# Kernel tuning notes

Measured on AMD Instinct MI355X. Metric: run time of the kernel, lower is better.

Reference implementation:

```python
import jax, jax.numpy as jnp
import numpy as np

N, F_IN, H1, H2 = 8192, 512, 256, 128
EPS_VAR = 1e-6


def setup_inputs() -> dict:
    key = jax.random.key(0)
    ks = jax.random.split(key, 12)
    rn = lambda k, s, sc=1.0: jax.random.normal(k, s, dtype=jnp.float32) * sc
    x = rn(ks[0], (N, F_IN))
    # dense normalized-adjacency surrogate: row sums ~0.5 keep activations bounded
    adj = jax.random.uniform(ks[1], (N, N), dtype=jnp.float32) / N
    g = lambda k, fi, fo: rn(k, (fi, fo), (1.0 / fi) ** 0.5)
    W1 = g(ks[2], F_IN, H1)
    W2 = g(ks[3], H1, H2)
    W3 = g(ks[4], H1, H2)
    W4 = g(ks[5], H1, H2)
    W5 = g(ks[6], H1, H2)
    Wl = g(ks[7], 2 * H2, H2)
    bl = jnp.zeros((H2,), jnp.float32)
    eps_z = rn(ks[8], (N, H2))          # eps for reparameterize (N(0,1))
    eps_group = rn(ks[9], (1, H2), 0.1)  # group eps ~ N(0, 0.1)
    batch = jnp.zeros((N,), jnp.int32)   # torch code uses all-ones labels -> one group
    return dict(x=x, adj=adj, W1=W1, W2=W2, W3=W3, W4=W4, W5=W5,
                Wl=Wl, bl=bl, eps_z=eps_z, eps_group=eps_group, batch=batch)


def _gcn(adj, h, W, act):
    return act(adj @ (h @ W))


def _accumulate_group_evidence(clz_mu, clz_logvar, batch):
    # precision-weighted group mean/var, vectorized segment reduce (1 group here)
    var = jnp.exp(clz_logvar)
    var = jnp.where(var == 0.0, EPS_VAR, var)
    inv = 1.0 / var                                             # [N,H2]
    prec = jax.ops.segment_sum(inv, batch, num_segments=1)      # [G,H2]
    gvar = 1.0 / prec
    gmu = gvar * jax.ops.segment_sum(clz_mu * inv, batch, num_segments=1)
    grouped_mu = gmu[batch]                                     # [N,H2]
    gv = gvar[batch]
    gv = jnp.where(gv == 0.0, EPS_VAR, gv)
    return grouped_mu, jnp.log(gv)


def reference(x, adj, W1, W2, W3, W4, W5, Wl, bl, eps_z, eps_group, batch):
    h1 = _gcn(adj, x, W1, jax.nn.relu)
    ident = lambda v: v
    mu = _gcn(adj, h1, W2, ident)
    logvar = _gcn(adj, h1, W3, ident)
    clz_mu = _gcn(adj, h1, W4, ident)
    clz_logvar = _gcn(adj, h1, W5, ident)

    # reparameterize: std = exp(logvar) in the original (no 0.5 factor)
    z = eps_z * jnp.exp(logvar) + mu

    # group evidence path uses .data in torch -> detached from encoder
    grouped_mu, grouped_logvar = _accumulate_group_evidence(
        jax.lax.stop_gradient(clz_mu), jax.lax.stop_gradient(clz_logvar), batch)

    # group-wise reparameterize: same eps per group, std = exp(0.5*logvar)
    class_lat = grouped_mu + jnp.exp(0.5 * grouped_logvar) * eps_group[batch]

    updated_z = jnp.concatenate([z, class_lat], axis=-1) @ Wl + bl  # [N,H2]
    adj_recon = updated_z @ updated_z.T                             # [N,N], act=identity
    return adj_recon, z, mu, logvar, grouped_mu, grouped_logvar
```

## Files before the change

### kernel.cpp

```cpp
#include <hip/hip_runtime.h>
#include <math.h>
#include <stdint.h>

namespace {

constexpr long OUT_ADJ = 0;
constexpr long OUT_Z   = 67108864;
constexpr long OUT_MU  = 68157440;
constexpr long OUT_LV  = 69206016;
constexpr long OUT_GMU = 70254592;
constexpr long OUT_GLV = 71303168;

constexpr long P_F32OFF    = 0;
constexpr long ADJBF_U16   = 16777216;
constexpr long Y1T_U16     = 83886080;
constexpr long H1T_U16     = 85983232;

constexpr long OFF_Y1    = 0;
constexpr long OFF_U     = 0;
constexpr long OFF_UBF   = 1048576;
constexpr long OFF_STATS = 1572864;
constexpr long OFF_G     = 2097152;
constexpr long OFF_M2    = 4194304;
constexpr long OFF_WCAT  = 8388608;

typedef short bf16x8 __attribute__((ext_vector_type(8)));
typedef float f32x4  __attribute__((ext_vector_type(4)));

__device__ __forceinline__ uint16_t f2bf(float f) {
    uint32_t u = __float_as_uint(f);
    return (uint16_t)((u + 0x7FFFu + ((u >> 16) & 1u)) >> 16);
}

__device__ __forceinline__ void gload16(const void* g, void* lds) {
    __builtin_amdgcn_global_load_lds(
        (__attribute__((address_space(1))) void*)(void*)g,
        (__attribute__((address_space(3))) void*)lds, 16, 0, 0);
}

__global__ __launch_bounds__(256)
void cast_bf16(const float* __restrict__ in, uint16_t* __restrict__ out, long n8) {
    long i = (long)blockIdx.x * 256 + threadIdx.x;
    if (i >= n8) return;
    const float4* p = (const float4*)in + i * 2;
    float4 a = p[0], b = p[1];
    union { uint16_t u[8]; uint4 v; } r;
    r.u[0] = f2bf(a.x); r.u[1] = f2bf(a.y); r.u[2] = f2bf(a.z); r.u[3] = f2bf(a.w);
    r.u[4] = f2bf(b.x); r.u[5] = f2bf(b.y); r.u[6] = f2bf(b.z); r.u[7] = f2bf(b.w);
    *(uint4*)(out + i * 8) = r.v;
}

__global__ __launch_bounds__(256)
void pack_wcat(const float* __restrict__ W2, const float* __restrict__ W3,
               const float* __restrict__ W4, const float* __restrict__ W5,
               float* __restrict__ Wcat) {
    int id = blockIdx.x * 256 + threadIdx.x;
    int k = id >> 9;
    int c = id & 511;
    int q = c >> 7, cc = c & 127;
    const float* W = (q == 0) ? W2 : (q == 1) ? W3 : (q == 2) ? W4 : W5;
    Wcat[id] = W[k * 128 + cc];
}

__global__ void init_stats(float* stats) {
    int t = threadIdx.x;
    if (t < 256) stats[t] = 0.f;
}

template<bool RELU, bool BIAS>
__global__ __launch_bounds__(256)
void gemm128x64(const float* __restrict__ A, const float* __restrict__ B,
                const float* __restrict__ bias, float* __restrict__ C,
                int M, int N, int K) {
    constexpr int SA = 132;
    constexpr int SB = 68;
    __shared__ float Ast[16 * SA];
    __shared__ float Bs[16 * SB];
    const int t  = threadIdx.x;
    const int tx = t & 15, ty = t >> 4;
    const long i0 = (long)blockIdx.x * 128;
    const long j0 = (long)blockIdx.y * 64;

    const int a_row = t >> 2;
    const int a_q   = (t & 3) << 2;
    const int b_k   = t >> 4;
    const int b_c   = (t & 15) << 2;

    const float* Ap0 = A + (i0 + a_row) * (long)K + a_q;
    const float* Ap1 = Ap0 + 64l * K;
    const float* Bp  = B + (long)b_k * N + j0 + b_c;

    float acc[8][4] = {};

    for (int kt = 0; kt < K; kt += 16) {
        float4 av0 = *(const float4*)(Ap0 + kt);
        float4 av1 = *(const float4*)(Ap1 + kt);
        float4 bv  = *(const float4*)(Bp + (long)kt * N);
        __syncthreads();
        Ast[(a_q + 0) * SA + a_row] = av0.x;
        Ast[(a_q + 1) * SA + a_row] = av0.y;
        Ast[(a_q + 2) * SA + a_row] = av0.z;
        Ast[(a_q + 3) * SA + a_row] = av0.w;
        Ast[(a_q + 0) * SA + a_row + 64] = av1.x;
        Ast[(a_q + 1) * SA + a_row + 64] = av1.y;
        Ast[(a_q + 2) * SA + a_row + 64] = av1.z;
        Ast[(a_q + 3) * SA + a_row + 64] = av1.w;
        *(float4*)&Bs[b_k * SB + b_c] = bv;
        __syncthreads();
        #pragma unroll
        for (int k = 0; k < 16; ++k) {
            float a[8], b[4];
            *(float4*)&a[0] = *(const float4*)&Ast[k * SA + ty * 8];
            *(float4*)&a[4] = *(const float4*)&Ast[k * SA + ty * 8 + 4];
            *(float4*)&b[0] = *(const float4*)&Bs[k * SB + tx * 4];
            #pragma unroll
            for (int ii = 0; ii < 8; ++ii)
                #pragma unroll
                for (int jj = 0; jj < 4; ++jj)
                    acc[ii][jj] = fmaf(a[ii], b[jj], acc[ii][jj]);
        }
    }

    #pragma unroll
    for (int ii = 0; ii < 8; ++ii) {
        long gi = i0 + ty * 8 + ii;
        float4 v;
        float* vp = &v.x;
        #pragma unroll
        for (int jj = 0; jj < 4; ++jj) {
            float xv = acc[ii][jj];
            if (BIAS) xv += bias[j0 + tx * 4 + jj];
            if (RELU) xv = fmaxf(xv, 0.f);
            vp[jj] = xv;
        }
        *(float4*)&C[gi * N + j0 + tx * 4] = v;
    }
}

__global__ __launch_bounds__(256)
void gemm_mfma_bt(const uint16_t* __restrict__ A, const uint16_t* __restrict__ BT,
                  float* __restrict__ P, int ldx, int Nout, int Ksplit) {
    __shared__ uint16_t sA[128 * 64];
    __shared__ uint16_t sB[128 * 64];
    const int t = threadIdx.x;
    const int l = t & 63, w = t >> 6;
    const int quad = l >> 4, l15 = l & 15;
    const long i0 = (long)blockIdx.x * 128;
    const long j0 = (long)blockIdx.y * 128;
    const int kbase = blockIdx.z * Ksplit;

    const uint16_t* gA[4];
    const uint16_t* gB[4];
    int dstb[4];
    #pragma unroll
    for (int q = 0; q < 4; ++q) {
        int cid = (q * 4 + w) * 64 + l;
        int row = cid >> 3;
        int cg  = (cid & 7) ^ (row & 7);
        gA[q] = A  + (i0 + row) * (long)ldx + kbase + cg * 8;
        gB[q] = BT + (j0 + row) * (long)ldx + kbase + cg * 8;
        dstb[q] = (q * 4 + w) * 1024;
    }

    const int wm = w & 1, wn = w >> 1;
    int offA[2][4], offB[2][4];
    #pragma unroll
    for (int ks = 0; ks < 2; ++ks) {
        int g = ks * 4 + quad;
        #pragma unroll
        for (int i = 0; i < 4; ++i) {
            int m = 64 * wm + 16 * i + l15;
            offA[ks][i] = m * 64 + ((g ^ (m & 7)) * 8);
            int n = 64 * wn + 16 * i + l15;
            offB[ks][i] = n * 64 + ((g ^ (n & 7)) * 8);
        }
    }

    f32x4 acc[4][4];
    #pragma unroll
    for (int i = 0; i < 4; ++i)
        #pragma unroll
        for (int j = 0; j < 4; ++j)
            acc[i][j] = (f32x4){0.f, 0.f, 0.f, 0.f};

    char* sAb = (char*)&sA[0];
    char* sBb = (char*)&sB[0];
    for (int kt = 0; kt < Ksplit; kt += 64) {
        __syncthreads();
        #pragma unroll
        for (int q = 0; q < 4; ++q) {
            gload16(gA[q] + kt, sAb + dstb[q]);
            gload16(gB[q] + kt, sBb + dstb[q]);
        }
        __syncthreads();
        #pragma unroll
        for (int ks = 0; ks < 2; ++ks) {
            bf16x8 af[4], bfr[4];
            #pragma unroll
            for (int mi = 0; mi < 4; ++mi) af[mi]  = *(const bf16x8*)&sA[offA[ks][mi]];
            #pragma unroll
            for (int ni = 0; ni < 4; ++ni) bfr[ni] = *(const bf16x8*)&sB[offB[ks][ni]];
            #pragma unroll
            for (int mi = 0; mi < 4; ++mi)
                #pragma unroll
                for (int ni = 0; ni < 4; ++ni)
                    acc[mi][ni] = __builtin_amdgcn_mfma_f32_16x16x32_bf16(
                        af[mi], bfr[ni], acc[mi][ni], 0, 0, 0);
        }
    }

    float* Pz = P + (long)blockIdx.z * (8192l * Nout);
    #pragma unroll
    for (int mi = 0; mi < 4; ++mi) {
        #pragma unroll
        for (int ni = 0; ni < 4; ++ni) {
            f32x4 v = acc[mi][ni];
            long col = j0 + 64 * wn + 16 * ni + l15;
            #pragma unroll
            for (int r = 0; r < 4; ++r) {
                long row = i0 + 64 * wm + 16 * mi + quad * 4 + r;
                Pz[row * Nout + col] = v[r];
            }
        }
    }
}

template<int NSUM, bool RELU>
__global__ __launch_bounds__(256)
void reduce_transpose_cast(const float* __restrict__ P, int M, int Ncols, long stride,
                           uint16_t* __restrict__ OT) {
    __shared__ float tile[64][65];
    long r0 = (long)blockIdx.x * 64;
    int  c0 = blockIdx.y * 64;
    int t = threadIdx.x;
    #pragma unroll
    for (int p = 0; p < 16; ++p) {
        int e = p * 256 + t;
        int r = e >> 6, c = e & 63;
        long idx = (r0 + r) * Ncols + c0 + c;
        float s = 0.f;
        #pragma unroll
        for (int q = 0; q < NSUM; ++q) s += P[idx + q * stride];
        if (RELU) s = fmaxf(s, 0.f);
        tile[r][c] = s;
    }
    __syncthreads();
    #pragma unroll
    for (int p = 0; p < 16; ++p) {
        int e = p * 256 + t;
        int c = e >> 6, r = e & 63;
        OT[(long)(c0 + c) * M + r0 + r] = f2bf(tile[r][c]);
    }
}

__global__ __launch_bounds__(256)
void reduce4(const float4* __restrict__ P, float4* __restrict__ G) {
    long i = (long)blockIdx.x * 256 + threadIdx.x;
    float4 a = P[i], b = P[i + 524288], c = P[i + 1048576], d = P[i + 1572864];
    float4 r;
    r.x = a.x + b.x + c.x + d.x;
    r.y = a.y + b.y + c.y + d.y;
    r.z = a.z + b.z + c.z + d.z;
    r.w = a.w + b.w + c.w + d.w;
    G[i] = r;
}

__global__ __launch_bounds__(128)
void group_reduce(const float* __restrict__ M2, float* __restrict__ stats) {
    int j = threadIdx.x;
    long base = (long)blockIdx.x * 32;
    float accP = 0.f, accS = 0.f;
    for (int r = 0; r < 32; ++r) {
        long i = base + r;
        float cmu = M2[i * 512 + 256 + j];
        float clv = M2[i * 512 + 384 + j];
        float var = expf(clv);
        if (var == 0.f) var = 1e-6f;
        float inv = 1.f / var;
        accP += inv;
        accS += cmu * inv;
    }
    atomicAdd(&stats[j], accP);
    atomicAdd(&stats[128 + j], accS);
}

__global__ __launch_bounds__(128)
void finalize_k(float* __restrict__ stats, const float* __restrict__ eps_group,
                const float* __restrict__ Wl, const float* __restrict__ bl) {
    __shared__ float cl[128];
    int j = threadIdx.x;
    float prec = stats[j];
    float s    = stats[128 + j];
    float gvar = 1.f / prec;
    float gmu  = gvar * s;
    float gv   = gvar; if (gv == 0.f) gv = 1e-6f;
    float glv  = logf(gv);
    stats[256 + j] = gmu;
    stats[384 + j] = glv;
    cl[j] = gmu + expf(0.5f * glv) * eps_group[j];
    __syncthreads();
    float c2 = bl[j];
    for (int k = 0; k < 128; ++k)
        c2 = fmaf(cl[k], Wl[(128 + k) * 128 + j], c2);
    stats[512 + j] = c2;
}

__global__ __launch_bounds__(256)
void epilogue_z(const float* __restrict__ M2, const float* __restrict__ eps_z,
                const float* __restrict__ stats, float* __restrict__ out) {
    long id = (long)blockIdx.x * 256 + threadIdx.x;
    long i = id >> 7;
    int  j = (int)(id & 127);
    float mu = M2[i * 512 + j];
    float lv = M2[i * 512 + 128 + j];
    out[OUT_Z   + id] = eps_z[id] * expf(lv) + mu;
    out[OUT_MU  + id] = mu;
    out[OUT_LV  + id] = lv;
    out[OUT_GMU + id] = stats[256 + j];
    out[OUT_GLV + id] = stats[384 + j];
}

__global__ __launch_bounds__(256)
void aat_mfma(const uint16_t* __restrict__ U, float* __restrict__ C) {
    __shared__ uint16_t sA[128 * 128];
    __shared__ uint16_t sB[128 * 128];
    const int t = threadIdx.x;
    const int l = t & 63, w = t >> 6;
    const int quad = l >> 4, l15 = l & 15;
    const long i0 = (long)blockIdx.x * 128;
    const long j0 = (long)blockIdx.y * 128;

    #pragma unroll
    for (int q = 0; q < 8; ++q) {
        int cid = (q * 4 + w) * 64 + l;
        int row = cid >> 4;
        int cg  = (cid & 15) ^ (row & 15);
        int dstb = (q * 4 + w) * 1024;
        gload16(U + (i0 + row) * 128 + cg * 8, (char*)&sA[0] + dstb);
        gload16(U + (j0 + row) * 128 + cg * 8, (char*)&sB[0] + dstb);
    }

    f32x4 acc[4][4];
    #pragma unroll
    for (int i = 0; i < 4; ++i)
        #pragma unroll
        for (int j = 0; j < 4; ++j)
            acc[i][j] = (f32x4){0.f, 0.f, 0.f, 0.f};

    __syncthreads();

    const int wm = w & 1, wn = w >> 1;
    #pragma unroll
    for (int ks = 0; ks < 4; ++ks) {
        int g = ks * 4 + quad;
        bf16x8 af[4], bfr[4];
        #pragma unroll
        for (int mi = 0; mi < 4; ++mi) {
            int m = 64 * wm + 16 * mi + l15;
            af[mi] = *(const bf16x8*)&sA[m * 128 + ((g ^ (m & 15)) * 8)];
        }
        #pragma unroll
        for (int ni = 0; ni < 4; ++ni) {
            int n = 64 * wn + 16 * ni + l15;
            bfr[ni] = *(const bf16x8*)&sB[n * 128 + ((g ^ (n & 15)) * 8)];
        }
        #pragma unroll
        for (int mi = 0; mi < 4; ++mi)
            #pragma unroll
            for (int ni = 0; ni < 4; ++ni)
                acc[mi][ni] = __builtin_amdgcn_mfma_f32_16x16x32_bf16(
                    af[mi], bfr[ni], acc[mi][ni], 0, 0, 0);
    }

    #pragma unroll
    for (int mi = 0; mi < 4; ++mi) {
        #pragma unroll
        for (int ni = 0; ni < 4; ++ni) {
            f32x4 v = acc[mi][ni];
            long col = j0 + 64 * wn + 16 * ni + l15;
            #pragma unroll
            for (int r = 0; r < 4; ++r) {
                long row = i0 + 64 * wm + 16 * mi + quad * 4 + r;
                C[row * 8192 + col] = v[r];
            }
        }
    }
}

}

extern "C" void kernel_launch(void* const* d_in, const int* in_sizes, int n_in,
                              void* d_out, int out_size, void* d_ws, size_t ws_size,
                              hipStream_t stream) {
    (void)in_sizes; (void)n_in; (void)out_size; (void)ws_size;
    const float* x     = (const float*)d_in[0];
    const float* adj   = (const float*)d_in[1];
    const float* W1    = (const float*)d_in[2];
    const float* W2    = (const float*)d_in[3];
    const float* W3    = (const float*)d_in[4];
    const float* W4    = (const float*)d_in[5];
    const float* W5    = (const float*)d_in[6];
    const float* Wl    = (const float*)d_in[7];
    const float* bl    = (const float*)d_in[8];
    const float* eps_z = (const float*)d_in[9];
    const float* eps_g = (const float*)d_in[10];

    float*    out  = (float*)d_out;
    uint16_t* outu = (uint16_t*)d_out;
    float*    ws   = (float*)d_ws;

    float*    P     = out + P_F32OFF;
    uint16_t* adjbf = outu + ADJBF_U16;
    uint16_t* Y1T   = outu + Y1T_U16;
    uint16_t* h1T   = outu + H1T_U16;

    float*    Y1  = ws + OFF_Y1;
    float*    U   = ws + OFF_U;
    uint16_t* Ubf = (uint16_t*)(ws + OFF_UBF);
    float*    st  = ws + OFF_STATS;
    float*    G   = ws + OFF_G;
    float*    M2  = ws + OFF_M2;
    float*    Wc  = ws + OFF_WCAT;

    cast_bf16<<<32768, 256, 0, stream>>>(adj, adjbf, 8388608);
    pack_wcat<<<512, 256, 0, stream>>>(W2, W3, W4, W5, Wc);
    init_stats<<<1, 256, 0, stream>>>(st);

    gemm128x64<false, false><<<dim3(64, 4), 256, 0, stream>>>(x, W1, nullptr, Y1, 8192, 256, 512);
    reduce_transpose_cast<1, false><<<dim3(128, 4), 256, 0, stream>>>(Y1, 8192, 256, 0, Y1T);

    gemm_mfma_bt<<<dim3(64, 2, 4), 256, 0, stream>>>(adjbf, Y1T, P, 8192, 256, 2048);
    reduce_transpose_cast<4, true><<<dim3(128, 4), 256, 0, stream>>>(P, 8192, 256, 2097152, h1T);

    gemm_mfma_bt<<<dim3(64, 2, 4), 256, 0, stream>>>(adjbf, h1T, P, 8192, 256, 2048);
    reduce4<<<2048, 256, 0, stream>>>((const float4*)P, (float4*)G);

    gemm128x64<false, false><<<dim3(64, 8), 256, 0, stream>>>(G, Wc, nullptr, M2, 8192, 512, 256);

    group_reduce<<<256, 128, 0, stream>>>(M2, st);
    finalize_k<<<1, 128, 0, stream>>>(st, eps_g, Wl, bl);
    epilogue_z<<<4096, 256, 0, stream>>>(M2, eps_z, st, out);

    gemm128x64<false, true><<<dim3(64, 2), 256, 0, stream>>>(out + OUT_Z, Wl, st + 512, U, 8192, 128, 128);
    cast_bf16<<<512, 256, 0, stream>>>(U, Ubf, 131072);

    aat_mfma<<<dim3(64, 64), 256, 0, stream>>>(Ubf, out);
}
```

Baseline: 791.6 us.

## Replace fp32 SIMT GEMMs with bf16 MFMA GEMMs and fuse weight prep

The three small fp32 FMA GEMMs (x@W1, G@Wcat, z@Wl) become instances of the bf16 MFMA kernel, which gains epilogue modes for transposed bf16 output and bias plus bf16 output. Weight transposes/casts, the x cast and the stats init are merged into one prep kernel. The reduce and epilogue kernels now emit bf16 directly, removing the separate transpose-cast and cast passes. These GEMMs are small next to the adjacency GEMMs, so the overall gain is limited, and bf16 inputs add rounding error to mu/logvar and the reconstruction.

Result: faster. 693.5 us (-12.4%).

```diff
diff --git a/kernel.cpp b/kernel.cpp
--- a/kernel.cpp
+++ b/kernel.cpp
@@ -15,14 +15,16 @@
 constexpr long ADJBF_U16   = 16777216;
 constexpr long Y1T_U16     = 83886080;
 constexpr long H1T_U16     = 85983232;
-
-constexpr long OFF_Y1    = 0;
-constexpr long OFF_U     = 0;
+constexpr long XBF_U16     = 88080384;
+constexpr long GBF_U16     = 92274688;
+constexpr long ZBF_U16     = 94371840;
+constexpr long W1T_U16     = 95420416;
+constexpr long WCT_U16     = 95551488;
+constexpr long WLT_U16     = 95682560;
+
 constexpr long OFF_UBF   = 1048576;
 constexpr long OFF_STATS = 1572864;
-constexpr long OFF_G     = 2097152;
 constexpr long OFF_M2    = 4194304;
-constexpr long OFF_WCAT  = 8388608;
 
 typedef short bf16x8 __attribute__((ext_vector_type(8)));
 typedef float f32x4  __attribute__((ext_vector_type(4)));
@@ -51,95 +53,48 @@
 }
 
 __global__ __launch_bounds__(256)
-void pack_wcat(const float* __restrict__ W2, const float* __restrict__ W3,
-               const float* __restrict__ W4, const float* __restrict__ W5,
-               float* __restrict__ Wcat) {
-    int id = blockIdx.x * 256 + threadIdx.x;
-    int k = id >> 9;
-    int c = id & 511;
-    int q = c >> 7, cc = c & 127;
-    const float* W = (q == 0) ? W2 : (q == 1) ? W3 : (q == 2) ? W4 : W5;
-    Wcat[id] = W[k * 128 + cc];
-}
-
-__global__ void init_stats(float* stats) {
+void prep_small(const float* __restrict__ x, const float* __restrict__ W1,
+                const float* __restrict__ W2, const float* __restrict__ W3,
+                const float* __restrict__ W4, const float* __restrict__ W5,
+                const float* __restrict__ Wl,
+                uint16_t* __restrict__ xbf, uint16_t* __restrict__ W1T,
+                uint16_t* __restrict__ WcT, uint16_t* __restrict__ WlT,
+                float* __restrict__ stats) {
+    int b = blockIdx.x;
     int t = threadIdx.x;
-    if (t < 256) stats[t] = 0.f;
-}
-
-template<bool RELU, bool BIAS>
-__global__ __launch_bounds__(256)
-void gemm128x64(const float* __restrict__ A, const float* __restrict__ B,
-                const float* __restrict__ bias, float* __restrict__ C,
-                int M, int N, int K) {
-    constexpr int SA = 132;
-    constexpr int SB = 68;
-    __shared__ float Ast[16 * SA];
-    __shared__ float Bs[16 * SB];
-    const int t  = threadIdx.x;
-    const int tx = t & 15, ty = t >> 4;
-    const long i0 = (long)blockIdx.x * 128;
-    const long j0 = (long)blockIdx.y * 64;
-
-    const int a_row = t >> 2;
-    const int a_q   = (t & 3) << 2;
-    const int b_k   = t >> 4;
-    const int b_c   = (t & 15) << 2;
-
-    const float* Ap0 = A + (i0 + a_row) * (long)K + a_q;
-    const float* Ap1 = Ap0 + 64l * K;
-    const float* Bp  = B + (long)b_k * N + j0 + b_c;
-
-    float acc[8][4] = {};
-
-    for (int kt = 0; kt < K; kt += 16) {
-        float4 av0 = *(const float4*)(Ap0 + kt);
-        float4 av1 = *(const float4*)(Ap1 + kt);
-        float4 bv  = *(const float4*)(Bp + (long)kt * N);
-        __syncthreads();
-        Ast[(a_q + 0) * SA + a_row] = av0.x;
-        Ast[(a_q + 1) * SA + a_row] = av0.y;
-        Ast[(a_q + 2) * SA + a_row] = av0.z;
-        Ast[(a_q + 3) * SA + a_row] = av0.w;
-        Ast[(a_q + 0) * SA + a_row + 64] = av1.x;
-        Ast[(a_q + 1) * SA + a_row + 64] = av1.y;
-        Ast[(a_q + 2) * SA + a_row + 64] = av1.z;
-        Ast[(a_q + 3) * SA + a_row + 64] = av1.w;
-        *(float4*)&Bs[b_k * SB + b_c] = bv;
-        __syncthreads();
-        #pragma unroll
-        for (int k = 0; k < 16; ++k) {
-            float a[8], b[4];
-            *(float4*)&a[0] = *(const float4*)&Ast[k * SA + ty * 8];
-            *(float4*)&a[4] = *(const float4*)&Ast[k * SA + ty * 8 + 4];
-            *(float4*)&b[0] = *(const float4*)&Bs[k * SB + tx * 4];
-            #pragma unroll
-            for (int ii = 0; ii < 8; ++ii)
-                #pragma unroll
-                for (int jj = 0; jj < 4; ++jj)
-                    acc[ii][jj] = fmaf(a[ii], b[jj], acc[ii][jj]);
-        }
-    }
-
-    #pragma unroll
-    for (int ii = 0; ii < 8; ++ii) {
-        long gi = i0 + ty * 8 + ii;
-        float4 v;
-        float* vp = &v.x;
-        #pragma unroll
-        for (int jj = 0; jj < 4; ++jj) {
-            float xv = acc[ii][jj];
-            if (BIAS) xv += bias[j0 + tx * 4 + jj];
-            if (RELU) xv = fmaxf(xv, 0.f);
-            vp[jj] = xv;
-        }
-        *(float4*)&C[gi * N + j0 + tx * 4] = v;
-    }
-}
-
+    if (b < 2048) {
+        long i = (long)b * 256 + t;
+        const float4* p = (const float4*)x + i * 2;
+        float4 a = p[0], c = p[1];
+        union { uint16_t u[8]; uint4 v; } r;
+        r.u[0] = f2bf(a.x); r.u[1] = f2bf(a.y); r.u[2] = f2bf(a.z); r.u[3] = f2bf(a.w);
+        r.u[4] = f2bf(c.x); r.u[5] = f2bf(c.y); r.u[6] = f2bf(c.z); r.u[7] = f2bf(c.w);
+        *(uint4*)(xbf + i * 8) = r.v;
+    } else if (b < 2048 + 512) {
+        int id = (b - 2048) * 256 + t;
+        int j = id >> 9, k = id & 511;
+        W1T[id] = f2bf(W1[(long)k * 256 + j]);
+    } else if (b < 2048 + 512 + 512) {
+        int id = (b - 2048 - 512) * 256 + t;
+        int c = id >> 8, k = id & 255;
+        int q = c >> 7, cc = c & 127;
+        const float* W = (q == 0) ? W2 : (q == 1) ? W3 : (q == 2) ? W4 : W5;
+        WcT[id] = f2bf(W[(long)k * 128 + cc]);
+    } else if (b < 2048 + 512 + 512 + 64) {
+        int id = (b - 2048 - 1024) * 256 + t;
+        int j = id >> 7, k = id & 127;
+        WlT[id] = f2bf(Wl[(long)k * 128 + j]);
+    } else {
+        if (t < 256) stats[t] = 0.f;
+    }
+}
+
+template<int MODE>
 __global__ __launch_bounds__(256)
 void gemm_mfma_bt(const uint16_t* __restrict__ A, const uint16_t* __restrict__ BT,
-                  float* __restrict__ P, int ldx, int Nout, int Ksplit) {
+                  float* __restrict__ P, uint16_t* __restrict__ O,
+                  const float* __restrict__ bias,
+                  int ldx, int Nout, int Ksplit) {
     __shared__ uint16_t sA[128 * 64];
     __shared__ uint16_t sB[128 * 64];
     const int t = threadIdx.x;
@@ -209,17 +164,47 @@
         }
     }
 
-    float* Pz = P + (long)blockIdx.z * (8192l * Nout);
-    #pragma unroll
-    for (int mi = 0; mi < 4; ++mi) {
-        #pragma unroll
-        for (int ni = 0; ni < 4; ++ni) {
-            f32x4 v = acc[mi][ni];
-            long col = j0 + 64 * wn + 16 * ni + l15;
-            #pragma unroll
-            for (int r = 0; r < 4; ++r) {
-                long row = i0 + 64 * wm + 16 * mi + quad * 4 + r;
-                Pz[row * Nout + col] = v[r];
+    if (MODE == 0) {
+        float* Pz = P + (long)blockIdx.z * (8192l * Nout);
+        #pragma unroll
+        for (int mi = 0; mi < 4; ++mi) {
+            #pragma unroll
+            for (int ni = 0; ni < 4; ++ni) {
+                f32x4 v = acc[mi][ni];
+                long col = j0 + 64 * wn + 16 * ni + l15;
+                #pragma unroll
+                for (int r = 0; r < 4; ++r) {
+                    long row = i0 + 64 * wm + 16 * mi + quad * 4 + r;
+                    Pz[row * Nout + col] = v[r];
+                }
+            }
+        }
+    } else if (MODE == 1) {
+        #pragma unroll
+        for (int mi = 0; mi < 4; ++mi) {
+            long rowb = i0 + 64 * wm + 16 * mi + quad * 4;
+            #pragma unroll
+            for (int ni = 0; ni < 4; ++ni) {
+                f32x4 v = acc[mi][ni];
+                long col = j0 + 64 * wn + 16 * ni + l15;
+                union { uint16_t u[4]; uint2 q2; } r4;
+                r4.u[0] = f2bf(v[0]); r4.u[1] = f2bf(v[1]);
+                r4.u[2] = f2bf(v[2]); r4.u[3] = f2bf(v[3]);
+                *(uint2*)&O[col * 8192 + rowb] = r4.q2;
+            }
+        }
+    } else {
+        #pragma unroll
+        for (int mi = 0; mi < 4; ++mi) {
+            long rowb = i0 + 64 * wm + 16 * mi + quad * 4;
+            #pragma unroll
+            for (int ni = 0; ni < 4; ++ni) {
+                f32x4 v = acc[mi][ni];
+                long col = j0 + 64 * wn + 16 * ni + l15;
+                float bv = bias[col];
+                #pragma unroll
+                for (int r = 0; r < 4; ++r)
+                    O[(rowb + r) * Nout + col] = f2bf(v[r] + bv);
             }
         }
     }
@@ -254,15 +239,21 @@
 }
 
 __global__ __launch_bounds__(256)
-void reduce4(const float4* __restrict__ P, float4* __restrict__ G) {
+void reduce4_bf16(const float4* __restrict__ P, uint16_t* __restrict__ G) {
     long i = (long)blockIdx.x * 256 + threadIdx.x;
-    float4 a = P[i], b = P[i + 524288], c = P[i + 1048576], d = P[i + 1572864];
-    float4 r;
-    r.x = a.x + b.x + c.x + d.x;
-    r.y = a.y + b.y + c.y + d.y;
-    r.z = a.z + b.z + c.z + d.z;
-    r.w = a.w + b.w + c.w + d.w;
-    G[i] = r;
+    long b = i * 2;
+    float4 s0 = {0.f,0.f,0.f,0.f}, s1 = {0.f,0.f,0.f,0.f};
+    #pragma unroll
+    for (int q = 0; q < 4; ++q) {
+        float4 a = P[b + q * 524288];
+        float4 c = P[b + 1 + q * 524288];
+        s0.x += a.x; s0.y += a.y; s0.z += a.z; s0.w += a.w;
+        s1.x += c.x; s1.y += c.y; s1.z += c.z; s1.w += c.w;
+    }
+    union { uint16_t u[8]; uint4 v; } r;
+    r.u[0] = f2bf(s0.x); r.u[1] = f2bf(s0.y); r.u[2] = f2bf(s0.z); r.u[3] = f2bf(s0.w);
+    r.u[4] = f2bf(s1.x); r.u[5] = f2bf(s1.y); r.u[6] = f2bf(s1.z); r.u[7] = f2bf(s1.w);
+    *(uint4*)(G + i * 8) = r.v;
 }
 
 __global__ __launch_bounds__(128)
@@ -307,17 +298,20 @@
 
 __global__ __launch_bounds__(256)
 void epilogue_z(const float* __restrict__ M2, const float* __restrict__ eps_z,
-                const float* __restrict__ stats, float* __restrict__ out) {
+                const float* __restrict__ stats, float* __restrict__ out,
+                uint16_t* __restrict__ zbf) {
     long id = (long)blockIdx.x * 256 + threadIdx.x;
     long i = id >> 7;
     int  j = (int)(id & 127);
     float mu = M2[i * 512 + j];
     float lv = M2[i * 512 + 128 + j];
-    out[OUT_Z   + id] = eps_z[id] * expf(lv) + mu;
+    float z  = eps_z[id] * expf(lv) + mu;
+    out[OUT_Z   + id] = z;
     out[OUT_MU  + id] = mu;
     out[OUT_LV  + id] = lv;
     out[OUT_GMU + id] = stats[256 + j];
     out[OUT_GLV + id] = stats[384 + j];
+    zbf[id] = f2bf(z);
 }
 
 __global__ __launch_bounds__(256)
@@ -413,36 +407,41 @@
     uint16_t* adjbf = outu + ADJBF_U16;
     uint16_t* Y1T   = outu + Y1T_U16;
     uint16_t* h1T   = outu + H1T_U16;
-
-    float*    Y1  = ws + OFF_Y1;
-    float*    U   = ws + OFF_U;
+    uint16_t* xbf   = outu + XBF_U16;
+    uint16_t* Gbf   = outu + GBF_U16;
+    uint16_t* zbf   = outu + ZBF_U16;
+    uint16_t* W1T   = outu + W1T_U16;
+    uint16_t* WcT   = outu + WCT_U16;
+    uint16_t* WlT   = outu + WLT_U16;
+
     uint16_t* Ubf = (uint16_t*)(ws + OFF_UBF);
     float*    st  = ws + OFF_STATS;
-    float*    G   = ws + OFF_G;
     float*    M2  = ws + OFF_M2;
-    float*    Wc  = ws + OFF_WCAT;
 
     cast_bf16<<<32768, 256, 0, stream>>>(adj, adjbf, 8388608);
-    pack_wcat<<<512, 256, 0, stream>>>(W2, W3, W4, W5, Wc);
-    init_stats<<<1, 256, 0, stream>>>(st);
-
-    gemm128x64<false, false><<<dim3(64, 4), 256, 0, stream>>>(x, W1, nullptr, Y1, 8192, 256, 512);
-    reduce_transpose_cast<1, false><<<dim3(128, 4), 256, 0, stream>>>(Y1, 8192, 256, 0, Y1T);
-
-    gemm_mfma_bt<<<dim3(64, 2, 4), 256, 0, stream>>>(adjbf, Y1T, P, 8192, 256, 2048);
+    prep_small<<<3137, 256, 0, stream>>>(x, W1, W2, W3, W4, W5, Wl,
+                                         xbf, W1T, WcT, WlT, st);
+
+    gemm_mfma_bt<1><<<dim3(64, 2, 1), 256, 0, stream>>>(
+        xbf, W1T, nullptr, Y1T, nullptr, 512, 256, 512);
+
+    gemm_mfma_bt<0><<<dim3(64, 2, 4), 256, 0, stream>>>(
+        adjbf, Y1T, P, nullptr, nullptr, 8192, 256, 2048);
     reduce_transpose_cast<4, true><<<dim3(128, 4), 256, 0, stream>>>(P, 8192, 256, 2097152, h1T);
 
-    gemm_mfma_bt<<<dim3(64, 2, 4), 256, 0, stream>>>(adjbf, h1T, P, 8192, 256, 2048);
-    reduce4<<<2048, 256, 0, stream>>>((const float4*)P, (float4*)G);
-
-    gemm128x64<false, false><<<dim3(64, 8), 256, 0, stream>>>(G, Wc, nullptr, M2, 8192, 512, 256);
+    gemm_mfma_bt<0><<<dim3(64, 2, 4), 256, 0, stream>>>(
+        adjbf, h1T, P, nullptr, nullptr, 8192, 256, 2048);
+    reduce4_bf16<<<1024, 256, 0, stream>>>((const float4*)P, Gbf);
+
+    gemm_mfma_bt<0><<<dim3(64, 4, 1), 256, 0, stream>>>(
+        Gbf, WcT, M2, nullptr, nullptr, 256, 512, 256);
 
     group_reduce<<<256, 128, 0, stream>>>(M2, st);
     finalize_k<<<1, 128, 0, stream>>>(st, eps_g, Wl, bl);
-    epilogue_z<<<4096, 256, 0, stream>>>(M2, eps_z, st, out);
-
-    gemm128x64<false, true><<<dim3(64, 2), 256, 0, stream>>>(out + OUT_Z, Wl, st + 512, U, 8192, 128, 128);
-    cast_bf16<<<512, 256, 0, stream>>>(U, Ubf, 131072);
+    epilogue_z<<<4096, 256, 0, stream>>>(M2, eps_z, st, out, zbf);
+
+    gemm_mfma_bt<2><<<dim3(64, 1, 1), 256, 0, stream>>>(
+        zbf, WlT, nullptr, Ubf, st + 512, 128, 128, 128);
 
     aat_mfma<<<dim3(64, 64), 256, 0, stream>>>(Ubf, out);
 }
```
